# Performance work log

Hardware: AMD Instinct MI355X
Metric: run time of the kernel (lower is better)

## Reference

```python
import jax, jax.numpy as jnp
import numpy as np

N_NODES = 50000
N_EDGES = 800000
NEG_SLOPE = 0.2  # DGL GATConv default LeakyReLU slope


def _gat_layer(h, src, dst, W, attn_l, attn_r, bias, activation):
    """One DGL-style GATConv (eval mode, no dropout).
    h: [N, Din]; W: [Din, H*F]; attn_l/attn_r: [H, F]; bias: [H*F].
    Returns [N, H, F].
    """
    H, F = attn_l.shape
    feat = (h @ W).reshape(-1, H, F)                      # [N, H, F]
    el = jnp.sum(feat * attn_l[None], axis=-1)            # [N, H]
    er = jnp.sum(feat * attn_r[None], axis=-1)            # [N, H]
    e = jax.nn.leaky_relu(el[src] + er[dst], NEG_SLOPE)   # [E, H]
    # segment softmax over incoming edges of each dst node
    m = jax.ops.segment_max(e, dst, num_segments=N_NODES)  # [N, H]
    ex = jnp.exp(e - m[dst])                               # [E, H]
    s = jax.ops.segment_sum(ex, dst, num_segments=N_NODES)  # [N, H]
    alpha = ex / s[dst]                                    # [E, H]
    msg = feat[src] * alpha[..., None]                     # [E, H, F]
    out = jax.ops.segment_sum(msg, dst, num_segments=N_NODES)  # [N, H, F]
    out = out + bias.reshape(1, H, F)
    if activation is not None:
        out = activation(out)
    return out


def setup_inputs() -> dict:
    key = jax.random.key(0)
    ks = jax.random.split(key, 16)
    in_size, hid, h0, h2, out_size = 256, 16, 8, 1, 64
    d1 = hid * h0  # 128
    inp = {
        "x": jax.random.normal(ks[0], (N_NODES, in_size), dtype=jnp.float32),
        "src": jax.random.randint(ks[1], (N_EDGES,), 0, N_NODES, dtype=jnp.int32),
        "dst": jax.random.randint(ks[2], (N_EDGES,), 0, N_NODES, dtype=jnp.int32),
        "W0": jax.random.normal(ks[3], (in_size, h0 * hid), dtype=jnp.float32) * 0.1,
        "al0": jax.random.normal(ks[4], (h0, hid), dtype=jnp.float32) * 0.1,
        "ar0": jax.random.normal(ks[5], (h0, hid), dtype=jnp.float32) * 0.1,
        "b0": jnp.zeros((h0 * hid,), dtype=jnp.float32),
        "W1": jax.random.normal(ks[6], (d1, h0 * hid), dtype=jnp.float32) * 0.1,
        "al1": jax.random.normal(ks[7], (h0, hid), dtype=jnp.float32) * 0.1,
        "ar1": jax.random.normal(ks[8], (h0, hid), dtype=jnp.float32) * 0.1,
        "b1": jnp.zeros((h0 * hid,), dtype=jnp.float32),
        "W2": jax.random.normal(ks[9], (d1, h2 * out_size), dtype=jnp.float32) * 0.1,
        "al2": jax.random.normal(ks[10], (h2, out_size), dtype=jnp.float32) * 0.1,
        "ar2": jax.random.normal(ks[11], (h2, out_size), dtype=jnp.float32) * 0.1,
        "b2": jnp.zeros((h2 * out_size,), dtype=jnp.float32),
    }
    return inp


def reference(x, src, dst, W0, al0, ar0, b0, W1, al1, ar1, b1, W2, al2, ar2, b2):
    elu = jax.nn.elu
    h = _gat_layer(x, src, dst, W0, al0, ar0, b0, elu)      # [N, 8, 16]
    h = h.reshape(h.shape[0], -1)                           # flatten heads -> [N, 128]
    h = _gat_layer(h, src, dst, W1, al1, ar1, b1, elu)      # [N, 8, 16]
    h = h.reshape(h.shape[0], -1)                           # [N, 128]
    h = _gat_layer(h, src, dst, W2, al2, ar2, b2, None)     # [N, 1, 64]
    return h.mean(axis=1)                                   # [N, 64]
```

## Files before the change

kernel.cpp:

```cpp
#include <hip/hip_runtime.h>
#include <hip/hip_bf16.h>
#include <hip/hip_fp16.h>
#include <cstdint>

#define N_NODES 50000
#define N_EDGES 800000

typedef _Float16 half8_t __attribute__((ext_vector_type(8)));
typedef float f32x4 __attribute__((ext_vector_type(4)));

template<int DIN, int DOUT, int F>
__global__ void prepack_w(const float* __restrict__ W, const float* __restrict__ al,
                          const float* __restrict__ ar, __half* __restrict__ Wp)
{
    constexpr int NKS = DIN / 32;
    constexpr int NT  = DOUT / 16;
    constexpr int H   = DOUT / F;
    int f = blockIdx.x * blockDim.x + threadIdx.x;
    if (f >= (NT + 1) * NKS * 64) return;
    int lane = f & 63;
    int ks   = (f >> 6) % NKS;
    int nt   = (f >> 6) / NKS;
    int kbase = ks * 32 + (lane >> 4) * 8;
    int n = lane & 15;
    __half h[8];
    if (nt < NT) {
#pragma unroll
        for (int j = 0; j < 8; ++j)
            h[j] = __float2half(W[(size_t)(kbase + j) * DOUT + nt * 16 + n]);
    } else {
#pragma unroll
        for (int j = 0; j < 8; ++j) {
            float s = 0.f;
            if (n < H) {
                for (int ff = 0; ff < F; ++ff)
                    s += W[(size_t)(kbase + j) * DOUT + n * F + ff] * al[n * F + ff];
            } else if (n < 2 * H) {
                int hh = n - H;
                for (int ff = 0; ff < F; ++ff)
                    s += W[(size_t)(kbase + j) * DOUT + hh * F + ff] * ar[hh * F + ff];
            }
            h[j] = __float2half(s);
        }
    }
    *reinterpret_cast<uint4*>(&Wp[(size_t)f * 8]) = *reinterpret_cast<uint4*>(h);
}

template<int DIN, int DOUT, int F>
__global__ __launch_bounds__(256) void gemm_attn_mfma(
    const float* __restrict__ X, const __half* __restrict__ Wp,
    __half* __restrict__ feat, float* __restrict__ el, float* __restrict__ er, int N)
{
    constexpr int NKS = DIN / 32;
    constexpr int NT  = DOUT / 16;
    constexpr int NTT = NT + 1;
    constexpr int H   = DOUT / F;

    const int wid  = threadIdx.x >> 6;
    const int lane = threadIdx.x & 63;
    const int row0 = blockIdx.x * 64 + wid * 16;
    const int m    = lane & 15;
    const int kg   = lane >> 4;

    const int rowa = min(row0 + m, N - 1);
    const float* Xr = X + (size_t)rowa * DIN + kg * 8;

    f32x4 acc[NTT];
#pragma unroll
    for (int i = 0; i < NTT; ++i) acc[i] = (f32x4){0.f, 0.f, 0.f, 0.f};

    float4 xa = *reinterpret_cast<const float4*>(Xr);
    float4 xb = *reinterpret_cast<const float4*>(Xr + 4);

#pragma unroll
    for (int ks = 0; ks < NKS; ++ks) {
        float4 xan = xa, xbn = xb;
        if (ks + 1 < NKS) {
            xan = *reinterpret_cast<const float4*>(Xr + (ks + 1) * 32);
            xbn = *reinterpret_cast<const float4*>(Xr + (ks + 1) * 32 + 4);
        }
        half8_t a;
        a[0] = (_Float16)xa.x; a[1] = (_Float16)xa.y;
        a[2] = (_Float16)xa.z; a[3] = (_Float16)xa.w;
        a[4] = (_Float16)xb.x; a[5] = (_Float16)xb.y;
        a[6] = (_Float16)xb.z; a[7] = (_Float16)xb.w;
#pragma unroll
        for (int nt = 0; nt < NTT; ++nt) {
            const half8_t b = *reinterpret_cast<const half8_t*>(
                Wp + ((size_t)(nt * NKS + ks) * 64 + lane) * 8);
            acc[nt] = __builtin_amdgcn_mfma_f32_16x16x32_f16(a, b, acc[nt], 0, 0, 0);
        }
        xa = xan; xb = xbn;
    }

    const int q = lane >> 4;
#pragma unroll
    for (int reg = 0; reg < 4; ++reg) {
        const int row = row0 + 4 * q + reg;
        if (row < N) {
#pragma unroll
            for (int nt = 0; nt < NT; ++nt)
                feat[(size_t)row * DOUT + nt * 16 + m] = __float2half(acc[nt][reg]);
            const float v = acc[NT][reg];
            if (m < H)          el[(size_t)row * H + m] = v;
            else if (m < 2 * H) er[(size_t)row * H + (m - H)] = v;
        }
    }
}

__global__ void zero_ints(int* __restrict__ a, int n)
{
    int i = blockIdx.x * blockDim.x + threadIdx.x;
    if (i < n) a[i] = 0;
}

__global__ void hist_deg(const int* __restrict__ dst, int* __restrict__ deg)
{
    int e = blockIdx.x * blockDim.x + threadIdx.x;
    if (e < N_EDGES) atomicAdd(&deg[dst[e]], 1);
}

__global__ __launch_bounds__(1024) void scan_partials(
    const int* __restrict__ deg, int* __restrict__ btot, int n)
{
    __shared__ int wsum[16];
    const int tid = threadIdx.x;
    const int lane = tid & 63, wid = tid >> 6;
    int i = blockIdx.x * 1024 + tid;
    int v = (i < n) ? deg[i] : 0;
#pragma unroll
    for (int off = 1; off < 64; off <<= 1) v += __shfl_xor(v, off);
    if (lane == 0) wsum[wid] = v;
    __syncthreads();
    if (tid < 16) {
        int w = wsum[tid];
#pragma unroll
        for (int off = 1; off < 16; off <<= 1) w += __shfl_xor(w, off, 16);
        if (tid == 0) btot[blockIdx.x] = w;
    }
}

__global__ void scan_btot(int* __restrict__ btot, int nb)
{
    int tid = threadIdx.x;
    int v = (tid < nb) ? btot[tid] : 0;
    int x = v;
#pragma unroll
    for (int off = 1; off < 64; off <<= 1) {
        int t = __shfl_up(x, off);
        if (tid >= off) x += t;
    }
    if (tid < nb) btot[tid] = x - v;
}

__global__ __launch_bounds__(1024) void scan_final(
    const int* __restrict__ deg, const int* __restrict__ bcar,
    int* __restrict__ offs, int n)
{
    __shared__ int wtot[16], wincl[16];
    const int tid = threadIdx.x;
    const int lane = tid & 63, wid = tid >> 6;
    int i = blockIdx.x * 1024 + tid;
    int v = (i < n) ? deg[i] : 0;
    int x = v;
#pragma unroll
    for (int off = 1; off < 64; off <<= 1) {
        int t = __shfl_up(x, off);
        if (lane >= off) x += t;
    }
    if (lane == 63) wtot[wid] = x;
    __syncthreads();
    if (tid < 16) {
        int wx = wtot[tid];
#pragma unroll
        for (int off = 1; off < 16; off <<= 1) {
            int t = __shfl_up(wx, off, 16);
            if (tid >= off) wx += t;
        }
        wincl[tid] = wx;
    }
    __syncthreads();
    int waveExcl = (wid == 0) ? 0 : wincl[wid - 1];
    if (i < n) offs[i] = bcar[blockIdx.x] + waveExcl + (x - v);
    if (i == 0) offs[n] = N_EDGES;
}

__global__ void build_csr(const int* __restrict__ src, const int* __restrict__ dst,
                          const int* __restrict__ offs, int* __restrict__ cursor,
                          int* __restrict__ csr_src)
{
    int e = blockIdx.x * blockDim.x + threadIdx.x;
    if (e >= N_EDGES) return;
    int d = dst[e];
    int p = offs[d] + atomicAdd(&cursor[d], 1);
    csr_src[p] = src[e];
}

template<int H, int F, bool ACT>
__global__ __launch_bounds__(256) void node_flash_agg(
    const int* __restrict__ offs, const int* __restrict__ csr_src,
    const float* __restrict__ el, const float* __restrict__ er,
    const __half* __restrict__ feat, const float* __restrict__ bias,
    float* __restrict__ out, int N)
{
    constexpr int D = H * F;
    constexpr int CPT = D / 64;
    constexpr int EPC = 64 / H;
    constexpr int MAXCH = (H == 8) ? 4 : 1;
    constexpr int SB = 8;
    constexpr int NB = MAXCH * EPC / SB;

    const int wid = threadIdx.x >> 6;
    const int lane = threadIdx.x & 63;
    const int n = blockIdx.x * 4 + wid;
    if (n >= N) return;

    const int beg = offs[n];
    const int deg = offs[n + 1] - beg;

    const int comp0 = CPT * lane;
    const int myhead = comp0 / F;

    if (deg == 0) {
#pragma unroll
        for (int c = 0; c < CPT; ++c) {
            float v = bias[comp0 + c];
            if (ACT) v = (v > 0.f) ? v : (__expf(v) - 1.f);
            out[(size_t)n * D + comp0 + c] = v;
        }
        return;
    }

    const int h = lane % H;
    const int esub = lane / H;
    const float erd = er[(size_t)n * H + h];

    float acc[CPT];
#pragma unroll
    for (int c = 0; c < CPT; ++c) acc[c] = 0.f;

    if (deg <= MAXCH * EPC) {
        const int nch = (deg + EPC - 1) / EPC;
        int sreg[MAXCH];
        float ex[MAXCH];

#pragma unroll
        for (int j = 0; j < MAXCH; ++j) {
            if (j < nch) {
                sreg[j] = csr_src[beg + min(j * EPC + esub, deg - 1)];
                ex[j] = el[(size_t)sreg[j] * H + h];
            }
        }
        float m = -1e30f;
#pragma unroll
        for (int j = 0; j < MAXCH; ++j) {
            if (j < nch) {
                float v = ex[j] + erd;
                v = (v > 0.f) ? v : 0.2f * v;
                v = (j * EPC + esub < deg) ? v : -1e30f;
                ex[j] = v;
                m = fmaxf(m, v);
            }
        }
#pragma unroll
        for (int off = H; off < 64; off <<= 1)
            m = fmaxf(m, __shfl_xor(m, off));
        float s = 0.f;
#pragma unroll
        for (int j = 0; j < MAXCH; ++j) {
            if (j < nch) { ex[j] = __expf(ex[j] - m); s += ex[j]; }
        }
#pragma unroll
        for (int off = H; off < 64; off <<= 1)
            s += __shfl_xor(s, off);
        const float inv = 1.f / s;
#pragma unroll
        for (int j = 0; j < MAXCH; ++j)
            if (j < nch) ex[j] *= inv;

        float fvA[SB][CPT], fvB[SB][CPT];
        auto ldb = [&](int j, int g, float (&fv)[SB][CPT]) {
#pragma unroll
            for (int ii = 0; ii < SB; ++ii) {
                int sl = __shfl(sreg[j], (g + ii) * H);
                if constexpr (CPT == 2) {
                    const __half2 t = *reinterpret_cast<const __half2*>(
                        &feat[(size_t)sl * D + comp0]);
                    const float2 f = __half22float2(t);
                    fv[ii][0] = f.x; fv[ii][1] = f.y;
                } else {
                    fv[ii][0] = __half2float(feat[(size_t)sl * D + comp0]);
                }
            }
        };
        auto fmab = [&](int j, int g, float (&fv)[SB][CPT]) {
#pragma unroll
            for (int ii = 0; ii < SB; ++ii) {
                float exb = __shfl(ex[j], (g + ii) * H + myhead);
#pragma unroll
                for (int c = 0; c < CPT; ++c)
                    acc[c] = fmaf(fv[ii][c], exb, acc[c]);
            }
        };

        ldb(0, 0, fvA);
#pragma unroll
        for (int b = 0; b < NB; ++b) {
            if (b * SB < deg) {
                if ((b + 1) * SB < deg) {
                    const int jn = ((b + 1) * SB) / EPC;
                    const int gn = ((b + 1) * SB) % EPC;
                    if ((b & 1) == 0) ldb(jn, gn, fvB);
                    else              ldb(jn, gn, fvA);
                }
                const int j = (b * SB) / EPC;
                const int g = (b * SB) % EPC;
                if ((b & 1) == 0) fmab(j, g, fvA);
                else              fmab(j, g, fvB);
            }
        }
#pragma unroll
        for (int c = 0; c < CPT; ++c) {
            float v = acc[c] + bias[comp0 + c];
            if (ACT) v = (v > 0.f) ? v : (__expf(v) - 1.f);
            acc[c] = v;
        }
    } else {
        float m_run = -1e30f, s_run = 0.f;
        int sN = csr_src[beg + min(esub, deg - 1)];
        float elN = el[(size_t)sN * H + h];

        for (int base = 0; base < deg; base += EPC) {
            const int s_mine = sN;
            const float elv = elN;
            const int nb = base + EPC;
            if (nb < deg) {
                sN = csr_src[beg + min(nb + esub, deg - 1)];
                elN = el[(size_t)sN * H + h];
            }
            float v = elv + erd;
            v = (v > 0.f) ? v : 0.2f * v;
            float logit = (base + esub < deg) ? v : -1e30f;

            float cmax = logit;
#pragma unroll
            for (int off = H; off < 64; off <<= 1)
                cmax = fmaxf(cmax, __shfl_xor(cmax, off));
            float nm = fmaxf(m_run, cmax);
            float scale = __expf(m_run - nm);
            float ex = __expf(logit - nm);
            float csum = ex;
#pragma unroll
            for (int off = H; off < 64; off <<= 1)
                csum += __shfl_xor(csum, off);
            s_run = s_run * scale + csum;
            m_run = nm;

            const float sc = __shfl(scale, myhead);
#pragma unroll
            for (int c = 0; c < CPT; ++c) acc[c] *= sc;

            const int active = min(EPC, deg - base);
            for (int g = 0; g < active; g += SB) {
                float fv[SB][CPT];
#pragma unroll
                for (int ii = 0; ii < SB; ++ii) {
                    int sl = __shfl(s_mine, (g + ii) * H);
                    if constexpr (CPT == 2) {
                        const __half2 t = *reinterpret_cast<const __half2*>(
                            &feat[(size_t)sl * D + comp0]);
                        const float2 f = __half22float2(t);
                        fv[ii][0] = f.x; fv[ii][1] = f.y;
                    } else {
                        fv[ii][0] = __half2float(feat[(size_t)sl * D + comp0]);
                    }
                }
#pragma unroll
                for (int ii = 0; ii < SB; ++ii) {
                    float exb = __shfl(ex, (g + ii) * H + myhead);
#pragma unroll
                    for (int c = 0; c < CPT; ++c)
                        acc[c] = fmaf(fv[ii][c], exb, acc[c]);
                }
            }
        }
        const float invb = __shfl(1.f / s_run, myhead);
#pragma unroll
        for (int c = 0; c < CPT; ++c) {
            float v = acc[c] * invb + bias[comp0 + c];
            if (ACT) v = (v > 0.f) ? v : (__expf(v) - 1.f);
            acc[c] = v;
        }
    }

    if constexpr (CPT == 2) {
        *reinterpret_cast<float2*>(&out[(size_t)n * D + comp0]) =
            make_float2(acc[0], acc[1]);
    } else {
        out[(size_t)n * D + comp0] = acc[0];
    }
}

extern "C" void kernel_launch(void* const* d_in, const int* in_sizes, int n_in,
                              void* d_out, int out_size, void* d_ws, size_t ws_size,
                              hipStream_t stream)
{
    const float* x   = (const float*)d_in[0];
    const int*   src = (const int*)d_in[1];
    const int*   dst = (const int*)d_in[2];
    const float* W0  = (const float*)d_in[3];
    const float* al0 = (const float*)d_in[4];
    const float* ar0 = (const float*)d_in[5];
    const float* b0  = (const float*)d_in[6];
    const float* W1  = (const float*)d_in[7];
    const float* al1 = (const float*)d_in[8];
    const float* ar1 = (const float*)d_in[9];
    const float* b1  = (const float*)d_in[10];
    const float* W2  = (const float*)d_in[11];
    const float* al2 = (const float*)d_in[12];
    const float* ar2 = (const float*)d_in[13];
    const float* b2  = (const float*)d_in[14];
    float* out = (float*)d_out;

    const int N = N_NODES, E = N_EDGES;

    const size_t wp0_h = 9 * 8 * 64 * 8;
    const size_t wp1_h = 9 * 4 * 64 * 8;
    const size_t wp2_h = 5 * 4 * 64 * 8;

    __half* Wp0 = (__half*)d_ws;
    __half* Wp1 = Wp0 + wp0_h;
    __half* Wp2 = Wp1 + wp1_h;
    float* fbase = (float*)(Wp2 + wp2_h + 2048);

    __half* feat = (__half*)fbase;
    float* hbuf = fbase + (size_t)N * 64;
    float* elb  = hbuf + (size_t)N * 128;
    float* erb  = elb + (size_t)N * 8;
    int* ibase   = (int*)(erb + (size_t)N * 8);
    int* deg     = ibase;
    int* cursor  = deg + N;
    int* offs    = cursor + N;
    int* csr_src = offs + N + 1;
    int* btot    = csr_src + E;

    const int TB = 256;
    const int gb_rows64 = (N + 63) / 64;
    const int gb_edges  = (E + TB - 1) / TB;
    const int gb_nodes  = (N + 3) / 4;
    const int nsb       = (N + 1023) / 1024;

    prepack_w<256, 128, 16><<<(9 * 8 * 64 + TB - 1) / TB, TB, 0, stream>>>(W0, al0, ar0, Wp0);
    prepack_w<128, 128, 16><<<(9 * 4 * 64 + TB - 1) / TB, TB, 0, stream>>>(W1, al1, ar1, Wp1);
    prepack_w<128, 64, 64><<<(5 * 4 * 64 + TB - 1) / TB, TB, 0, stream>>>(W2, al2, ar2, Wp2);

    zero_ints<<<(2 * N + TB - 1) / TB, TB, 0, stream>>>(deg, 2 * N);
    hist_deg<<<gb_edges, TB, 0, stream>>>(dst, deg);
    scan_partials<<<nsb, 1024, 0, stream>>>(deg, btot, N);
    scan_btot<<<1, 64, 0, stream>>>(btot, nsb);
    scan_final<<<nsb, 1024, 0, stream>>>(deg, btot, offs, N);
    build_csr<<<gb_edges, TB, 0, stream>>>(src, dst, offs, cursor, csr_src);

    gemm_attn_mfma<256, 128, 16><<<gb_rows64, 256, 0, stream>>>(x, Wp0, feat, elb, erb, N);
    node_flash_agg<8, 16, true><<<gb_nodes, 256, 0, stream>>>(
        offs, csr_src, elb, erb, feat, b0, hbuf, N);

    gemm_attn_mfma<128, 128, 16><<<gb_rows64, 256, 0, stream>>>(hbuf, Wp1, feat, elb, erb, N);
    node_flash_agg<8, 16, true><<<gb_nodes, 256, 0, stream>>>(
        offs, csr_src, elb, erb, feat, b1, hbuf, N);

    gemm_attn_mfma<128, 64, 64><<<gb_rows64, 256, 0, stream>>>(hbuf, Wp2, feat, elb, erb, N);
    node_flash_agg<1, 64, false><<<gb_nodes, 256, 0, stream>>>(
        offs, csr_src, elb, erb, feat, b2, out, N);
}
```

Baseline: 297.1 us.

## Partition CSR build by destination range and pre-seed cursors with offsets

```diff
diff --git a/kernel.cpp b/kernel.cpp
--- a/kernel.cpp
+++ b/kernel.cpp
@@ -155,7 +155,7 @@
 
 __global__ __launch_bounds__(1024) void scan_final(
     const int* __restrict__ deg, const int* __restrict__ bcar,
-    int* __restrict__ offs, int n)
+    int* __restrict__ offs, int* __restrict__ cursor, int n)
 {
     __shared__ int wtot[16], wincl[16];
     const int tid = threadIdx.x;
@@ -181,19 +181,38 @@
     }
     __syncthreads();
     int waveExcl = (wid == 0) ? 0 : wincl[wid - 1];
-    if (i < n) offs[i] = bcar[blockIdx.x] + waveExcl + (x - v);
+    if (i < n) {
+        int o = bcar[blockIdx.x] + waveExcl + (x - v);
+        offs[i] = o;
+        cursor[i] = o;
+    }
     if (i == 0) offs[n] = N_EDGES;
 }
 
-__global__ void build_csr(const int* __restrict__ src, const int* __restrict__ dst,
-                          const int* __restrict__ offs, int* __restrict__ cursor,
-                          int* __restrict__ csr_src)
-{
-    int e = blockIdx.x * blockDim.x + threadIdx.x;
-    if (e >= N_EDGES) return;
-    int d = dst[e];
-    int p = offs[d] + atomicAdd(&cursor[d], 1);
-    csr_src[p] = src[e];
+__global__ __launch_bounds__(256) void build_csr_part(
+    const int* __restrict__ src, const int* __restrict__ dst,
+    int* __restrict__ cursor, int* __restrict__ csr_src)
+{
+    constexpr int RNG = N_NODES / 8;
+    constexpr int SS  = N_EDGES / 100;
+    const int g  = blockIdx.x & 7;
+    const int s  = blockIdx.x >> 3;
+    const int lo = g * RNG;
+    const int e0 = s * SS;
+
+    for (int q = threadIdx.x; q < SS / 4; q += 256) {
+        const int4 d = *reinterpret_cast<const int4*>(&dst[e0 + 4 * q]);
+#pragma unroll
+        for (int k = 0; k < 4; ++k) {
+            const int dv = (k == 0) ? d.x : (k == 1) ? d.y : (k == 2) ? d.z : d.w;
+            const unsigned r = (unsigned)(dv - lo);
+            if (r < (unsigned)RNG) {
+                int sv = src[e0 + 4 * q + k];
+                int p = atomicAdd(&cursor[dv], 1);
+                csr_src[p] = sv;
+            }
+        }
+    }
 }
 
 template<int H, int F, bool ACT>
@@ -454,12 +473,12 @@
     prepack_w<128, 128, 16><<<(9 * 4 * 64 + TB - 1) / TB, TB, 0, stream>>>(W1, al1, ar1, Wp1);
     prepack_w<128, 64, 64><<<(5 * 4 * 64 + TB - 1) / TB, TB, 0, stream>>>(W2, al2, ar2, Wp2);
 
-    zero_ints<<<(2 * N + TB - 1) / TB, TB, 0, stream>>>(deg, 2 * N);
+    zero_ints<<<(N + TB - 1) / TB, TB, 0, stream>>>(deg, N);
     hist_deg<<<gb_edges, TB, 0, stream>>>(dst, deg);
     scan_partials<<<nsb, 1024, 0, stream>>>(deg, btot, N);
     scan_btot<<<1, 64, 0, stream>>>(btot, nsb);
-    scan_final<<<nsb, 1024, 0, stream>>>(deg, btot, offs, N);
-    build_csr<<<gb_edges, TB, 0, stream>>>(src, dst, offs, cursor, csr_src);
+    scan_final<<<nsb, 1024, 0, stream>>>(deg, btot, offs, cursor, N);
+    build_csr_part<<<800, 256, 0, stream>>>(src, dst, cursor, csr_src);
 
     gemm_attn_mfma<256, 128, 16><<<gb_rows64, 256, 0, stream>>>(x, Wp0, feat, elb, erb, N);
     node_flash_agg<8, 16, true><<<gb_nodes, 256, 0, stream>>>(
```

Measured after the change: 291.2 us. -2.0%, faster.
